# Performance work log

Hardware: AMD Instinct MI355X
Metric: run time of the kernel (lower is better)

Reference implementation:

```python
import jax, jax.numpy as jnp
import numpy as np

HIDDEN = 1152
N_HEADS = 4
N_KV = 1
HEAD_DIM = 256
EPS = 1e-6
B, S = 4, 2048
ROPE_THETA = 1000000.0


def _rms_norm(x, w):
    # x: [..., D] float32; Gemma-style (1 + w) scale
    xf = x.astype(jnp.float32)
    inv = jax.lax.rsqrt(jnp.mean(xf * xf, axis=-1, keepdims=True) + EPS)
    return (xf * inv * (1.0 + w.astype(jnp.float32))).astype(x.dtype)


def _apply_rope(x, cos, sin):
    # x: [B, H, S, D]; cos/sin: [S, D/2]
    d2 = x.shape[-1] // 2
    x1, x2 = x[..., :d2], x[..., d2:]
    cos = cos[None, None, :, :]
    sin = sin[None, None, :, :]
    xr = x1 * cos - x2 * sin
    xi = x1 * sin + x2 * cos
    return jnp.concatenate([xr, xi], axis=-1).astype(x.dtype)


def setup_inputs() -> dict:
    key = jax.random.key(0)
    k_h, k_qkv, k_qn, k_kn, k_o = jax.random.split(key, 5)
    hidden_states = jax.random.normal(k_h, (B, S, HIDDEN), dtype=jnp.float32)
    # causal additive mask [1,1,S,S]
    neg = jnp.finfo(jnp.float32).min
    causal = jnp.tril(jnp.ones((S, S), dtype=bool))
    attention_mask = jnp.where(causal, 0.0, neg)[None, None, :, :].astype(jnp.float32)
    # RoPE tables (complex freqs_cis split into cos/sin)
    inv_freq = 1.0 / (ROPE_THETA ** (np.arange(0, HEAD_DIM, 2, dtype=np.float32) / HEAD_DIM))
    ang = np.arange(S, dtype=np.float32)[:, None] * inv_freq[None, :]
    freqs_cos = jnp.asarray(np.cos(ang))
    freqs_sin = jnp.asarray(np.sin(ang))
    qkv_out = (N_HEADS + 2 * N_KV) * HEAD_DIM
    scale = HIDDEN ** -0.5
    w_qkv = jax.random.normal(k_qkv, (HIDDEN, qkv_out), dtype=jnp.float32) * scale
    w_o = jax.random.normal(k_o, (N_HEADS * HEAD_DIM, HIDDEN), dtype=jnp.float32) * (N_HEADS * HEAD_DIM) ** -0.5
    q_norm_w = jax.random.normal(k_qn, (HEAD_DIM,), dtype=jnp.float32) * 0.02
    k_norm_w = jax.random.normal(k_kn, (HEAD_DIM,), dtype=jnp.float32) * 0.02
    return {
        "hidden_states": hidden_states,
        "attention_mask": attention_mask,
        "freqs_cos": freqs_cos,
        "freqs_sin": freqs_sin,
        "w_qkv": w_qkv,
        "q_norm_w": q_norm_w,
        "k_norm_w": k_norm_w,
        "w_o": w_o,
    }


def reference(hidden_states, attention_mask, freqs_cos, freqs_sin, w_qkv, q_norm_w, k_norm_w, w_o):
    b, s, _ = hidden_states.shape
    groups = N_HEADS // N_KV
    scaling = HEAD_DIM ** -0.5

    qkv = jnp.einsum("bsh,ho->bso", hidden_states, w_qkv)
    q_end = N_HEADS * HEAD_DIM
    k_end = q_end + N_KV * HEAD_DIM
    q = qkv[:, :, :q_end].reshape(b, s, N_HEADS, HEAD_DIM).transpose(0, 2, 1, 3)
    k = qkv[:, :, q_end:k_end].reshape(b, s, N_KV, HEAD_DIM).transpose(0, 2, 1, 3)
    v = qkv[:, :, k_end:].reshape(b, s, N_KV, HEAD_DIM).transpose(0, 2, 1, 3)

    q = _rms_norm(q, q_norm_w)
    k = _rms_norm(k, k_norm_w)

    q = _apply_rope(q, freqs_cos, freqs_sin)
    k = _apply_rope(k, freqs_cos, freqs_sin)

    if groups > 1:
        k = jnp.repeat(k, groups, axis=1)  # [B, H, S, D]
        v = jnp.repeat(v, groups, axis=1)

    scores = jnp.einsum("bhqd,bhkd->bhqk", q * scaling, k)
    scores = scores + attention_mask.astype(jnp.float32)
    probs = jax.nn.softmax(scores.astype(jnp.float32), axis=-1).astype(q.dtype)

    attn = jnp.einsum("bhqk,bhkd->bhqd", probs, v)
    attn = attn.transpose(0, 2, 1, 3).reshape(b, s, N_HEADS * HEAD_DIM)
    return jnp.einsum("bsf,fh->bsh", attn, w_o)
```

## Files before the change

kernel.cpp:

```cpp
#include <hip/hip_runtime.h>

typedef _Float16 f16;
typedef _Float16 f16x8 __attribute__((ext_vector_type(8)));
typedef _Float16 f16x4 __attribute__((ext_vector_type(4)));
typedef float f32x4 __attribute__((ext_vector_type(4)));

#define NH 4
#define HD 256
#define BB 4
#define SS 2048
#define HID 1152
#define QKV_N 1536
#define ODIM (NH * HD)

#define QKV16_OFF 0L
#define HID16_OFF 25165824L
#define OBUF_OFF 0L
#define OPART_OFF 16777216L
#define ML_OFF 44040192L
#define QB_OFF 50331648L
#define KB_OFF 67108864L
#define VT_OFF 71303168L
#define WQKVT_OFF 75497472L
#define WOT_OFF 79036416L

#define GLL16(gp, lp)                                                      \
  __builtin_amdgcn_global_load_lds(                                       \
      (const __attribute__((address_space(1))) char*)(gp),                \
      (__attribute__((address_space(3))) char*)(lp), 16, 0, 0)

__global__ __launch_bounds__(256) void cvt_f32_to_f16(
    const float* __restrict__ s, f16* __restrict__ d, long n) {
  long i = ((long)blockIdx.x * 256 + threadIdx.x) * 8;
  long stride = (long)gridDim.x * 256 * 8;
  for (; i < n; i += stride) {
    float4 a = *(const float4*)(s + i);
    float4 b = *(const float4*)(s + i + 4);
    f16x8 h = {(f16)a.x, (f16)a.y, (f16)a.z, (f16)a.w,
               (f16)b.x, (f16)b.y, (f16)b.z, (f16)b.w};
    *(f16x8*)(d + i) = h;
  }
}

template <typename ST>
__global__ __launch_bounds__(256) void transpose_cvt(
    const ST* __restrict__ src, long src_ld, long src_bs,
    f16* __restrict__ dst, long dst_ld, long dst_bs) {
  __shared__ float tile[32][33];
  src += (long)blockIdx.z * src_bs;
  dst += (long)blockIdx.z * dst_bs;
  int r0 = blockIdx.y * 32, c0 = blockIdx.x * 32;
  int tc = threadIdx.x & 31, tr = threadIdx.x >> 5;
#pragma unroll
  for (int i = 0; i < 4; ++i)
    tile[tr + i * 8][tc] = (float)src[(long)(r0 + tr + i * 8) * src_ld + c0 + tc];
  __syncthreads();
#pragma unroll
  for (int i = 0; i < 4; ++i)
    dst[(long)(c0 + tr + i * 8) * dst_ld + r0 + tc] = (f16)tile[tc][tr + i * 8];
}

template <typename CT>
__global__ __launch_bounds__(256, 3) void gemm_f16(
    const f16* __restrict__ A, const f16* __restrict__ Bt,
    CT* __restrict__ C, int K, int N) {
  __shared__ f16 As[128][64];
  __shared__ f16 Bs[128][64];
  int tid = threadIdx.x, wave = tid >> 6, lane = tid & 63;
  int l16 = lane & 15, lhi = lane >> 4;
  int wm = (wave >> 1) * 64, wn = (wave & 1) * 64;
  long bm = (long)blockIdx.x * 128, bn = (long)blockIdx.y * 128;
  f32x4 acc[4][4] = {};

  int srow = wave * 32 + (lane >> 3);
  int scol = (lane & 7) * 8;
  const f16* Ag = A + (bm + srow) * (long)K + scol;
  const f16* Bg = Bt + (bn + srow) * (long)K + scol;

  for (int k0 = 0; k0 < K; k0 += 64) {
#pragma unroll
    for (int i = 0; i < 4; ++i)
      GLL16(Ag + k0 + (long)i * 8 * K, &As[wave * 32 + i * 8][0]);
#pragma unroll
    for (int i = 0; i < 4; ++i)
      GLL16(Bg + k0 + (long)i * 8 * K, &Bs[wave * 32 + i * 8][0]);
    __syncthreads();
#pragma unroll
    for (int kb = 0; kb < 2; ++kb) {
      f16x8 af[4], bf[4];
#pragma unroll
      for (int i = 0; i < 4; ++i)
        af[i] = *(const f16x8*)&As[wm + i * 16 + l16][kb * 32 + lhi * 8];
#pragma unroll
      for (int j = 0; j < 4; ++j)
        bf[j] = *(const f16x8*)&Bs[wn + j * 16 + l16][kb * 32 + lhi * 8];
#pragma unroll
      for (int i = 0; i < 4; ++i)
#pragma unroll
        for (int j = 0; j < 4; ++j)
          acc[i][j] =
              __builtin_amdgcn_mfma_f32_16x16x32_f16(bf[j], af[i], acc[i][j], 0, 0, 0);
    }
    __syncthreads();
  }

#pragma unroll
  for (int i = 0; i < 4; ++i) {
    long m = bm + wm + i * 16 + l16;
#pragma unroll
    for (int j = 0; j < 4; ++j) {
      long n = bn + wn + j * 16 + lhi * 4;
      if constexpr (sizeof(CT) == 2) {
        f16x4 h = {(f16)acc[i][j][0], (f16)acc[i][j][1], (f16)acc[i][j][2],
                   (f16)acc[i][j][3]};
        *(f16x4*)&C[m * N + n] = h;
      } else {
        *(f32x4*)&C[m * N + n] = acc[i][j];
      }
    }
  }
}

__device__ __forceinline__ void norm_rope_store(
    const f16* __restrict__ x, const float* __restrict__ w,
    const float* __restrict__ fc, const float* __restrict__ fs,
    f16* __restrict__ dst, float scale, int lane) {
  float x0 = (float)x[lane], x1 = (float)x[lane + 64];
  float x2 = (float)x[lane + 128], x3 = (float)x[lane + 192];
  float ss = x0 * x0 + x1 * x1 + x2 * x2 + x3 * x3;
#pragma unroll
  for (int m = 1; m < 64; m <<= 1) ss += __shfl_xor(ss, m, 64);
  float inv = rsqrtf(ss * (1.0f / 256.0f) + 1e-6f);
  x0 *= inv * (1.0f + w[lane]);
  x1 *= inv * (1.0f + w[lane + 64]);
  x2 *= inv * (1.0f + w[lane + 128]);
  x3 *= inv * (1.0f + w[lane + 192]);
  float c0 = fc[lane], s0 = fs[lane], c1 = fc[lane + 64], s1 = fs[lane + 64];
  dst[lane]       = (f16)((x0 * c0 - x2 * s0) * scale);
  dst[lane + 64]  = (f16)((x1 * c1 - x3 * s1) * scale);
  dst[lane + 128] = (f16)((x0 * s0 + x2 * c0) * scale);
  dst[lane + 192] = (f16)((x1 * s1 + x3 * c1) * scale);
}

__global__ __launch_bounds__(256) void qkv_post(
    const f16* __restrict__ qkv, const float* __restrict__ qnw,
    const float* __restrict__ knw, const float* __restrict__ fcos,
    const float* __restrict__ fsin, f16* __restrict__ Q, f16* __restrict__ Kb) {
  long row = blockIdx.x;
  int b = (int)(row >> 11), s = (int)(row & 2047);
  int wave = threadIdx.x >> 6, lane = threadIdx.x & 63;
  const f16* base = qkv + row * QKV_N;
  const float* fc = fcos + (long)s * 128;
  const float* fs = fsin + (long)s * 128;
  norm_rope_store(base + wave * HD, qnw, fc, fs,
                  Q + ((long)(b * NH + wave) * SS + s) * HD, 0.0625f, lane);
  if (wave == 0)
    norm_rope_store(base + NH * HD, knw, fc, fs, Kb + row * HD, 1.0f, lane);
}

__global__ __launch_bounds__(256, 4) void attn_fwd(
    const f16* __restrict__ Q, const f16* __restrict__ Kb,
    const f16* __restrict__ Vt, f16* __restrict__ O,
    f16* __restrict__ Opart, float2* __restrict__ ml) {
  __shared__ f16 Klds[32 * 256];
  __shared__ f16 Vlds[256 * 32];
  __shared__ f16 Plds[4][16][40];
  int bid = blockIdx.x;
  int xcd = bid & 7, slotid = bid >> 3;
  int b = xcd >> 1, par = xcd & 1;
  int h = slotid >> 5, ithalf = slotid & 31;
  int it = ithalf * 2 + par;
  if (it >= 63) return;

  int qb, t0, t1, slot = 0;
  bool split;
  if (it < 11) {
    qb = it; t0 = 0; t1 = 2 * qb + 2; split = false;
  } else {
    int j = it - 11, c, nch, lbase;
    if (j < 22) {
      qb = 11 + (j >> 1); c = j & 1; nch = 2; lbase = (qb - 11) * 2;
    } else {
      int jj = j - 22, q3 = jj / 3;
      qb = 22 + q3; c = jj - q3 * 3; nch = 3; lbase = 22 + q3 * 3;
    }
    int tiles = 2 * qb + 2;
    t0 = tiles * c / nch;
    t1 = tiles * (c + 1) / nch;
    split = true;
    slot = (b * NH + h) * 52 + lbase + c;
  }
  int tid = threadIdx.x, wave = tid >> 6, lane = tid & 63;
  int l16 = lane & 15, lhi = lane >> 4;
  int q0 = qb * 64 + wave * 16;

  const f16* Kg = Kb + (long)b * SS * HD;
  const f16* Vg = Vt + (long)b * HD * SS;

  f16x8 qf[8];
  const f16* Qbase = Q + ((long)(b * NH + h) * SS + q0 + l16) * HD + lhi * 8;
#pragma unroll
  for (int kb = 0; kb < 8; ++kb) qf[kb] = *(const f16x8*)(Qbase + kb * 32);

  f32x4 o[16] = {};
  float m_i = -1e30f, l_i = 0.f;

  int kr = tid >> 5, kc16 = (tid & 31) * 16;
  int rv = tid >> 2, vc16 = (tid & 3) * 16;
  char* kls = (char*)Klds;
  char* vls = (char*)Vlds;
  int kwsw = kc16 ^ (kr << 4);
  int vwsw = vc16 ^ ((rv & 3) << 4);
  const char* krd = kls + l16 * 512;
  int kswz = (l16 & 7) << 4;
  const char* vrd = vls + l16 * 64 + ((lhi * 16) ^ ((l16 & 3) << 4));

  for (int t = t0; t < t1; ++t) {
    long kv0 = (long)t * 32;
    __syncthreads();
#pragma unroll
    for (int i = 0; i < 4; ++i) {
      uint4 kval = *(const uint4*)((const char*)(Kg + (kv0 + kr + 8 * i) * HD) + kc16);
      *(uint4*)(kls + (kr + 8 * i) * 512 + kwsw) = kval;
    }
#pragma unroll
    for (int i = 0; i < 4; ++i) {
      uint4 vval = *(const uint4*)((const char*)(Vg + (long)(rv + 64 * i) * SS + kv0) + vc16);
      *(uint4*)(vls + (rv + 64 * i) * 64 + vwsw) = vval;
    }
    __syncthreads();

    f32x4 sc[2] = {};
    __builtin_amdgcn_s_setprio(1);
#pragma unroll
    for (int kb = 0; kb < 8; ++kb) {
#pragma unroll
      for (int cf = 0; cf < 2; ++cf) {
        f16x8 kf = *(const f16x8*)(krd + cf * 8192 + ((kb * 64 + lhi * 16) ^ kswz));
        sc[cf] = __builtin_amdgcn_mfma_f32_16x16x32_f16(kf, qf[kb], sc[cf], 0, 0, 0);
      }
    }
    __builtin_amdgcn_s_setprio(0);

    float p[8];
    float mx = -1e30f;
    int qrow = q0 + l16;
    if (t >= 2 * qb) {
#pragma unroll
      for (int cf = 0; cf < 2; ++cf)
#pragma unroll
        for (int r = 0; r < 4; ++r) {
          int kv = (int)kv0 + cf * 16 + lhi * 4 + r;
          float s = (kv <= qrow) ? sc[cf][r] : -1e30f;
          p[cf * 4 + r] = s;
          mx = fmaxf(mx, s);
        }
    } else {
#pragma unroll
      for (int i = 0; i < 8; ++i) {
        float s = sc[i >> 2][i & 3];
        p[i] = s;
        mx = fmaxf(mx, s);
      }
    }
    mx = fmaxf(mx, __shfl_xor(mx, 16));
    mx = fmaxf(mx, __shfl_xor(mx, 32));
    float mn = fmaxf(m_i, mx);
    float scl = __expf(m_i - mn);
    float rs = 0.f;
#pragma unroll
    for (int i = 0; i < 8; ++i) {
      p[i] = __expf(p[i] - mn);
      rs += p[i];
    }
    rs += __shfl_xor(rs, 16);
    rs += __shfl_xor(rs, 32);
    l_i = l_i * scl + rs;
    m_i = mn;

#pragma unroll
    for (int cf = 0; cf < 2; ++cf) {
      f16x4 hp = {(f16)p[cf * 4], (f16)p[cf * 4 + 1], (f16)p[cf * 4 + 2],
                  (f16)p[cf * 4 + 3]};
      *(f16x4*)&Plds[wave][l16][cf * 16 + lhi * 4] = hp;
    }

    float s0 = __shfl(scl, lhi * 4 + 0);
    float s1 = __shfl(scl, lhi * 4 + 1);
    float s2 = __shfl(scl, lhi * 4 + 2);
    float s3 = __shfl(scl, lhi * 4 + 3);
#pragma unroll
    for (int nf = 0; nf < 16; ++nf) {
      o[nf][0] *= s0;
      o[nf][1] *= s1;
      o[nf][2] *= s2;
      o[nf][3] *= s3;
    }

    f16x8 pa = *(const f16x8*)&Plds[wave][l16][lhi * 8];
    __builtin_amdgcn_s_setprio(1);
#pragma unroll
    for (int nf = 0; nf < 16; ++nf) {
      f16x8 vf = *(const f16x8*)(vrd + nf * 1024);
      o[nf] = __builtin_amdgcn_mfma_f32_16x16x32_f16(pa, vf, o[nf], 0, 0, 0);
    }
    __builtin_amdgcn_s_setprio(0);
  }

  float inv = 1.0f / l_i;
  float i0 = __shfl(inv, lhi * 4 + 0);
  float i1 = __shfl(inv, lhi * 4 + 1);
  float i2 = __shfl(inv, lhi * 4 + 2);
  float i3 = __shfl(inv, lhi * 4 + 3);
  float ir[4] = {i0, i1, i2, i3};
  if (!split) {
#pragma unroll
    for (int r = 0; r < 4; ++r) {
      long srow = q0 + lhi * 4 + r;
      f16* Orow = O + ((long)b * SS + srow) * ODIM + h * HD + l16;
#pragma unroll
      for (int nf = 0; nf < 16; ++nf) Orow[nf * 16] = (f16)(o[nf][r] * ir[r]);
    }
  } else {
#pragma unroll
    for (int r = 0; r < 4; ++r) {
      int rloc = wave * 16 + lhi * 4 + r;
      f16* Prow = Opart + ((long)slot * 64 + rloc) * HD + l16;
#pragma unroll
      for (int nf = 0; nf < 16; ++nf) Prow[nf * 16] = (f16)(o[nf][r] * ir[r]);
    }
    if (lane < 16) {
      float2 v; v.x = m_i; v.y = l_i;
      ml[(long)slot * 64 + wave * 16 + lane] = v;
    }
  }
}

__global__ __launch_bounds__(256) void attn_combine(
    const f16* __restrict__ Opart, const float2* __restrict__ ml,
    f16* __restrict__ O) {
  int x = blockIdx.x, h = blockIdx.y, b = blockIdx.z;
  int qb = 11 + x;
  int nch = (qb < 22) ? 2 : 3;
  int lbase = (qb < 22) ? (qb - 11) * 2 : 22 + (qb - 22) * 3;
  long slot0 = (long)(b * NH + h) * 52 + lbase;
  int tid = threadIdx.x;
  int r = tid >> 2, d0 = (tid & 3) * 64;
  float m[3], l[3], w[3];
  float M = -1e30f;
#pragma unroll
  for (int c = 0; c < 3; ++c)
    if (c < nch) {
      float2 v = ml[(slot0 + c) * 64 + r];
      m[c] = v.x; l[c] = v.y;
      M = fmaxf(M, v.x);
    }
  float sum = 0.f;
#pragma unroll
  for (int c = 0; c < 3; ++c)
    if (c < nch) { w[c] = l[c] * __expf(m[c] - M); sum += w[c]; }
  float inv = 1.0f / sum;
#pragma unroll
  for (int c = 0; c < 3; ++c)
    if (c < nch) w[c] *= inv;
  f16* Orow = O + ((long)b * SS + qb * 64 + r) * ODIM + h * HD + d0;
#pragma unroll
  for (int i = 0; i < 8; ++i) {
    float acc[8] = {};
#pragma unroll
    for (int c = 0; c < 3; ++c)
      if (c < nch) {
        f16x8 xv = *(const f16x8*)(Opart + ((slot0 + c) * 64 + r) * HD + d0 + i * 8);
#pragma unroll
        for (int j = 0; j < 8; ++j) acc[j] += w[c] * (float)xv[j];
      }
    f16x8 z;
#pragma unroll
    for (int j = 0; j < 8; ++j) z[j] = (f16)acc[j];
    *(f16x8*)(Orow + i * 8) = z;
  }
}

extern "C" void kernel_launch(void* const* d_in, const int* in_sizes, int n_in,
                              void* d_out, int out_size, void* d_ws, size_t ws_size,
                              hipStream_t stream) {
  const float* hidden = (const float*)d_in[0];
  const float* fcos = (const float*)d_in[2];
  const float* fsin = (const float*)d_in[3];
  const float* wqkv = (const float*)d_in[4];
  const float* qnw = (const float*)d_in[5];
  const float* knw = (const float*)d_in[6];
  const float* wo = (const float*)d_in[7];
  float* out = (float*)d_out;

  char* ws = (char*)d_ws;
  f16* qkv16 = (f16*)(ws + QKV16_OFF);
  f16* hid16 = (f16*)(ws + HID16_OFF);
  f16* Obuf = (f16*)(ws + OBUF_OFF);
  f16* Opart = (f16*)(ws + OPART_OFF);
  float2* ml = (float2*)(ws + ML_OFF);
  f16* Qb = (f16*)(ws + QB_OFF);
  f16* Kb = (f16*)(ws + KB_OFF);
  f16* Vt = (f16*)(ws + VT_OFF);
  f16* wqkvt = (f16*)(ws + WQKVT_OFF);
  f16* wot = (f16*)(ws + WOT_OFF);

  cvt_f32_to_f16<<<2048, 256, 0, stream>>>(hidden, hid16, (long)BB * SS * HID);

  transpose_cvt<float><<<dim3(QKV_N / 32, HID / 32, 1), 256, 0, stream>>>(
      wqkv, QKV_N, 0, wqkvt, HID, 0);
  transpose_cvt<float><<<dim3(HID / 32, ODIM / 32, 1), 256, 0, stream>>>(
      wo, HID, 0, wot, ODIM, 0);

  gemm_f16<f16><<<dim3(BB * SS / 128, QKV_N / 128), 256, 0, stream>>>(
      hid16, wqkvt, qkv16, HID, QKV_N);

  qkv_post<<<dim3(BB * SS), 256, 0, stream>>>(qkv16, qnw, knw, fcos, fsin, Qb, Kb);

  transpose_cvt<f16><<<dim3(HD / 32, SS / 32, BB), 256, 0, stream>>>(
      qkv16 + 1280, QKV_N, (long)SS * QKV_N, Vt, SS, (long)HD * SS);

  attn_fwd<<<dim3(1024), 256, 0, stream>>>(Qb, Kb, Vt, Obuf, Opart, ml);
  attn_combine<<<dim3(21, NH, BB), 256, 0, stream>>>(Opart, ml, Obuf);

  gemm_f16<float><<<dim3(BB * SS / 128, HID / 128), 256, 0, stream>>>(
      Obuf, wot, out, ODIM, HID);
}
```

Measured before the change: 240.6 us.

## Prefetch K/V into registers, lazily rescale softmax, vectorize norm-rope, merge weight transposes

The attention kernel now loads the next K/V tile into registers while the current tile is processed, and its occupancy hint drops from 4 to 3 blocks per SM to make room for those registers. The online softmax skips rescaling the accumulator when the running max grows by no more than a threshold, cutting exp calls and multiplies. Norm+RoPE switches to vectorized loads and stores with a lane shuffle for the rotate half. The two weight transpose launches are merged into one. The extra registers may reduce occupancy, and lazy rescaling could change numerics.

```diff
diff --git a/kernel.cpp b/kernel.cpp
--- a/kernel.cpp
+++ b/kernel.cpp
@@ -40,6 +40,30 @@
                (f16)b.x, (f16)b.y, (f16)b.z, (f16)b.w};
     *(f16x8*)(d + i) = h;
   }
+}
+
+__global__ __launch_bounds__(256) void transpose_weights(
+    const float* __restrict__ w1, f16* __restrict__ d1,
+    const float* __restrict__ w2, f16* __restrict__ d2) {
+  __shared__ float tile[32][33];
+  const float* src;
+  f16* dst;
+  long sld, dld;
+  if (blockIdx.z == 0) {
+    src = w1; dst = d1; sld = QKV_N; dld = HID;
+  } else {
+    if (blockIdx.x >= HID / 32 || blockIdx.y >= ODIM / 32) return;
+    src = w2; dst = d2; sld = HID; dld = ODIM;
+  }
+  int r0 = blockIdx.y * 32, c0 = blockIdx.x * 32;
+  int tc = threadIdx.x & 31, tr = threadIdx.x >> 5;
+#pragma unroll
+  for (int i = 0; i < 4; ++i)
+    tile[tr + i * 8][tc] = src[(long)(r0 + tr + i * 8) * sld + c0 + tc];
+  __syncthreads();
+#pragma unroll
+  for (int i = 0; i < 4; ++i)
+    dst[(long)(c0 + tr + i * 8) * dld + r0 + tc] = (f16)tile[tc][tr + i * 8];
 }
 
 template <typename ST>
@@ -125,21 +149,30 @@
     const f16* __restrict__ x, const float* __restrict__ w,
     const float* __restrict__ fc, const float* __restrict__ fs,
     f16* __restrict__ dst, float scale, int lane) {
-  float x0 = (float)x[lane], x1 = (float)x[lane + 64];
-  float x2 = (float)x[lane + 128], x3 = (float)x[lane + 192];
-  float ss = x0 * x0 + x1 * x1 + x2 * x2 + x3 * x3;
+  int a = lane & 31, hi = lane >> 5;
+  int d0 = 4 * a + 128 * hi;
+  f16x4 xv = *(const f16x4*)(x + d0);
+  float xf[4];
+#pragma unroll
+  for (int j = 0; j < 4; ++j) xf[j] = (float)xv[j];
+  float ss = xf[0] * xf[0] + xf[1] * xf[1] + xf[2] * xf[2] + xf[3] * xf[3];
 #pragma unroll
   for (int m = 1; m < 64; m <<= 1) ss += __shfl_xor(ss, m, 64);
   float inv = rsqrtf(ss * (1.0f / 256.0f) + 1e-6f);
-  x0 *= inv * (1.0f + w[lane]);
-  x1 *= inv * (1.0f + w[lane + 64]);
-  x2 *= inv * (1.0f + w[lane + 128]);
-  x3 *= inv * (1.0f + w[lane + 192]);
-  float c0 = fc[lane], s0 = fs[lane], c1 = fc[lane + 64], s1 = fs[lane + 64];
-  dst[lane]       = (f16)((x0 * c0 - x2 * s0) * scale);
-  dst[lane + 64]  = (f16)((x1 * c1 - x3 * s1) * scale);
-  dst[lane + 128] = (f16)((x0 * s0 + x2 * c0) * scale);
-  dst[lane + 192] = (f16)((x1 * s1 + x3 * c1) * scale);
+  f32x4 wv = *(const f32x4*)(w + d0);
+#pragma unroll
+  for (int j = 0; j < 4; ++j) xf[j] *= inv * (1.0f + wv[j]);
+  float pf[4];
+#pragma unroll
+  for (int j = 0; j < 4; ++j) pf[j] = __shfl_xor(xf[j], 32, 64);
+  f32x4 c = *(const f32x4*)(fc + 4 * a);
+  f32x4 s = *(const f32x4*)(fs + 4 * a);
+  float sign = hi ? 1.0f : -1.0f;
+  f16x4 out;
+#pragma unroll
+  for (int j = 0; j < 4; ++j)
+    out[j] = (f16)((xf[j] * c[j] + sign * pf[j] * s[j]) * scale);
+  *(f16x4*)(dst + d0) = out;
 }
 
 __global__ __launch_bounds__(256) void qkv_post(
@@ -158,7 +191,7 @@
     norm_rope_store(base + NH * HD, knw, fc, fs, Kb + row * HD, 1.0f, lane);
 }
 
-__global__ __launch_bounds__(256, 4) void attn_fwd(
+__global__ __launch_bounds__(256, 3) void attn_fwd(
     const f16* __restrict__ Q, const f16* __restrict__ Kb,
     const f16* __restrict__ Vt, f16* __restrict__ O,
     f16* __restrict__ Opart, float2* __restrict__ ml) {
@@ -215,18 +248,34 @@
   int kswz = (l16 & 7) << 4;
   const char* vrd = vls + l16 * 64 + ((lhi * 16) ^ ((l16 & 3) << 4));
 
+  uint4 kreg[4], vreg[4];
+  {
+    long kv0p = (long)t0 * 32;
+#pragma unroll
+    for (int i = 0; i < 4; ++i)
+      kreg[i] = *(const uint4*)((const char*)(Kg + (kv0p + kr + 8 * i) * HD) + kc16);
+#pragma unroll
+    for (int i = 0; i < 4; ++i)
+      vreg[i] = *(const uint4*)((const char*)(Vg + (long)(rv + 64 * i) * SS + kv0p) + vc16);
+  }
+
   for (int t = t0; t < t1; ++t) {
     long kv0 = (long)t * 32;
     __syncthreads();
 #pragma unroll
-    for (int i = 0; i < 4; ++i) {
-      uint4 kval = *(const uint4*)((const char*)(Kg + (kv0 + kr + 8 * i) * HD) + kc16);
-      *(uint4*)(kls + (kr + 8 * i) * 512 + kwsw) = kval;
-    }
-#pragma unroll
-    for (int i = 0; i < 4; ++i) {
-      uint4 vval = *(const uint4*)((const char*)(Vg + (long)(rv + 64 * i) * SS + kv0) + vc16);
-      *(uint4*)(vls + (rv + 64 * i) * 64 + vwsw) = vval;
+    for (int i = 0; i < 4; ++i)
+      *(uint4*)(kls + (kr + 8 * i) * 512 + kwsw) = kreg[i];
+#pragma unroll
+    for (int i = 0; i < 4; ++i)
+      *(uint4*)(vls + (rv + 64 * i) * 64 + vwsw) = vreg[i];
+    if (t + 1 < t1) {
+      long kn = (long)(t + 1) * 32;
+#pragma unroll
+      for (int i = 0; i < 4; ++i)
+        kreg[i] = *(const uint4*)((const char*)(Kg + (kn + kr + 8 * i) * HD) + kc16);
+#pragma unroll
+      for (int i = 0; i < 4; ++i)
+        vreg[i] = *(const uint4*)((const char*)(Vg + (long)(rv + 64 * i) * SS + kn) + vc16);
     }
     __syncthreads();
 
@@ -265,36 +314,48 @@
     }
     mx = fmaxf(mx, __shfl_xor(mx, 16));
     mx = fmaxf(mx, __shfl_xor(mx, 32));
-    float mn = fmaxf(m_i, mx);
-    float scl = __expf(m_i - mn);
-    float rs = 0.f;
-#pragma unroll
-    for (int i = 0; i < 8; ++i) {
-      p[i] = __expf(p[i] - mn);
-      rs += p[i];
-    }
-    rs += __shfl_xor(rs, 16);
-    rs += __shfl_xor(rs, 32);
-    l_i = l_i * scl + rs;
-    m_i = mn;
+
+    if (__all(mx <= m_i + 8.f)) {
+      float rs = 0.f;
+#pragma unroll
+      for (int i = 0; i < 8; ++i) {
+        p[i] = __expf(p[i] - m_i);
+        rs += p[i];
+      }
+      rs += __shfl_xor(rs, 16);
+      rs += __shfl_xor(rs, 32);
+      l_i += rs;
+    } else {
+      float mn = fmaxf(m_i, mx);
+      float scl = __expf(m_i - mn);
+      float rs = 0.f;
+#pragma unroll
+      for (int i = 0; i < 8; ++i) {
+        p[i] = __expf(p[i] - mn);
+        rs += p[i];
+      }
+      rs += __shfl_xor(rs, 16);
+      rs += __shfl_xor(rs, 32);
+      l_i = l_i * scl + rs;
+      m_i = mn;
+      float s0 = __shfl(scl, lhi * 4 + 0);
+      float s1 = __shfl(scl, lhi * 4 + 1);
+      float s2 = __shfl(scl, lhi * 4 + 2);
+      float s3 = __shfl(scl, lhi * 4 + 3);
+#pragma unroll
+      for (int nf = 0; nf < 16; ++nf) {
+        o[nf][0] *= s0;
+        o[nf][1] *= s1;
+        o[nf][2] *= s2;
+        o[nf][3] *= s3;
+      }
+    }
 
 #pragma unroll
     for (int cf = 0; cf < 2; ++cf) {
       f16x4 hp = {(f16)p[cf * 4], (f16)p[cf * 4 + 1], (f16)p[cf * 4 + 2],
                   (f16)p[cf * 4 + 3]};
       *(f16x4*)&Plds[wave][l16][cf * 16 + lhi * 4] = hp;
-    }
-
-    float s0 = __shfl(scl, lhi * 4 + 0);
-    float s1 = __shfl(scl, lhi * 4 + 1);
-    float s2 = __shfl(scl, lhi * 4 + 2);
-    float s3 = __shfl(scl, lhi * 4 + 3);
-#pragma unroll
-    for (int nf = 0; nf < 16; ++nf) {
-      o[nf][0] *= s0;
-      o[nf][1] *= s1;
-      o[nf][2] *= s2;
-      o[nf][3] *= s3;
     }
 
     f16x8 pa = *(const f16x8*)&Plds[wave][l16][lhi * 8];
@@ -407,10 +468,8 @@
 
   cvt_f32_to_f16<<<2048, 256, 0, stream>>>(hidden, hid16, (long)BB * SS * HID);
 
-  transpose_cvt<float><<<dim3(QKV_N / 32, HID / 32, 1), 256, 0, stream>>>(
-      wqkv, QKV_N, 0, wqkvt, HID, 0);
-  transpose_cvt<float><<<dim3(HID / 32, ODIM / 32, 1), 256, 0, stream>>>(
-      wo, HID, 0, wot, ODIM, 0);
+  transpose_weights<<<dim3(QKV_N / 32, HID / 32, 2), 256, 0, stream>>>(
+      wqkv, wqkvt, wo, wot);
 
   gemm_f16<f16><<<dim3(BB * SS / 128, QKV_N / 128), 256, 0, stream>>>(
       hid16, wqkvt, qkv16, HID, QKV_N);
```

Result: slower. 528.5 us (+119.6%).
